# Performance work log

Hardware: AMD Instinct MI355X
Metric: run time of the kernel (lower is better)

The kernel has to match this reference:

```python
import jax, jax.numpy as jnp
import numpy as np

LOG2 = float(np.log(2.0))
CUTOFF = 10.0
N, E, H, F, G = 50000, 800000, 64, 64, 50


def ssp(x):
    # ShiftedSoftplus
    return jax.nn.softplus(x) - LOG2


def setup_inputs() -> dict:
    key = jax.random.key(0)
    ks = jax.random.split(key, 20)
    s = 0.05
    inp = {
        'x0': jax.random.normal(ks[0], (N, H), jnp.float32),
        'x1': jax.random.normal(ks[1], (N, H), jnp.float32),
        'edge_index0': jax.random.randint(ks[2], (2, E), 0, N, jnp.int32),
        'edge_index1': jax.random.randint(ks[3], (2, E), 0, N, jnp.int32),
        'edge_weight0': jax.random.uniform(ks[4], (E,), jnp.float32) * CUTOFF,
        'edge_weight1': jax.random.uniform(ks[5], (E,), jnp.float32) * CUTOFF,
        'edge_attr0': jax.random.uniform(ks[6], (E, G), jnp.float32),
        'edge_attr1': jax.random.uniform(ks[7], (E, G), jnp.float32),
        # shared filter MLP (num_gaussians -> num_filters -> num_filters)
        'mlp_w1': jax.random.normal(ks[8], (G, F), jnp.float32) * s,
        'mlp_b1': jnp.zeros((F,), jnp.float32),
        'mlp_w2': jax.random.normal(ks[9], (F, F), jnp.float32) * s,
        'mlp_b2': jnp.zeros((F,), jnp.float32),
        # per-edge-type CFConv lin1 (H->F, no bias) and lin2 (F->H, bias)
        'lin1_w0': jax.random.normal(ks[10], (H, F), jnp.float32) * s,
        'lin2_w0': jax.random.normal(ks[11], (F, H), jnp.float32) * s,
        'lin2_b0': jnp.zeros((H,), jnp.float32),
        'lin1_w1': jax.random.normal(ks[12], (H, F), jnp.float32) * s,
        'lin2_w1': jax.random.normal(ks[13], (F, H), jnp.float32) * s,
        'lin2_b1': jnp.zeros((H,), jnp.float32),
        # trailing shared linear H->H
        'lin_w': jax.random.normal(ks[14], (H, H), jnp.float32) * s,
        'lin_b': jnp.zeros((H,), jnp.float32),
    }
    return inp


def cfconv(x, ei, ew, ea, l1w, l2w, l2b, mw1, mb1, mw2, mb2):
    # cosine cutoff on distances
    C = 0.5 * (jnp.cos(ew * (jnp.pi / CUTOFF)) + 1.0)  # [E]
    # filter MLP on RBF edge attrs: Linear -> SSP -> Linear
    W = (ssp(ea @ mw1 + mb1) @ mw2 + mb2) * C[:, None]  # [E,F]
    xs = x @ l1w                                        # [N,F]
    msg = xs[ei[0]] * W                                 # gather src, modulate
    agg = jax.ops.segment_sum(msg, ei[1], num_segments=x.shape[0])  # scatter-sum to dst
    return agg @ l2w + l2b                              # [N,H]


def reference(x0, x1, edge_index0, edge_index1, edge_weight0, edge_weight1,
              edge_attr0, edge_attr1, mlp_w1, mlp_b1, mlp_w2, mlp_b2,
              lin1_w0, lin2_w0, lin2_b0, lin1_w1, lin2_w1, lin2_b1,
              lin_w, lin_b):
    h0 = cfconv(x0, edge_index0, edge_weight0, edge_attr0,
                lin1_w0, lin2_w0, lin2_b0, mlp_w1, mlp_b1, mlp_w2, mlp_b2)
    h1 = cfconv(x1, edge_index1, edge_weight1, edge_attr1,
                lin1_w1, lin2_w1, lin2_b1, mlp_w1, mlp_b1, mlp_w2, mlp_b2)
    out0 = ssp(h0) @ lin_w + lin_b
    out1 = ssp(h1) @ lin_w + lin_b
    return out0, out1
```

## Files before the change

kernel.cpp:

```cpp
#include <hip/hip_runtime.h>
#include <math.h>

#define HD 64
#define GD 50
#define HALF 32
#define PAD 36

__device__ __forceinline__ float ssp_f(float x) {
    float ax = __builtin_fabsf(x);
    float e  = __expf(-ax);
    float sp = fmaxf(x, 0.0f) + __logf(1.0f + e);
    return sp - 0.69314718055994531f;
}

__global__ void __launch_bounds__(256) xs_kernel(const float* __restrict__ x,
                                                 const float* __restrict__ w,
                                                 float* __restrict__ xs,
                                                 float* __restrict__ agg, int N) {
    int wv = threadIdx.x >> 6;
    int j  = threadIdx.x & 63;
    int n  = blockIdx.x * 4 + wv;
    __shared__ float xr[4][64];
    if (n < N) xr[wv][j] = x[(size_t)n * HD + j];
    __syncthreads();
    if (n >= N) return;
    float acc = 0.0f;
#pragma unroll
    for (int k = 0; k < HD; ++k)
        acc = fmaf(xr[wv][k], w[k * HD + j], acc);
    xs[(size_t)n * HD + j] = acc;
    agg[(size_t)n * HD + j] = 0.0f;
}

#define EPW 64
#define WPB 2
__global__ void __launch_bounds__(WPB * 64, 4) edge_kernel(
        const float* __restrict__ ea, const float* __restrict__ ew,
        const int* __restrict__ ei, const float* __restrict__ xs,
        float* __restrict__ agg,
        const float* __restrict__ mw1, const float* __restrict__ mb1,
        const float* __restrict__ mw2, const float* __restrict__ mb2,
        int E) {
    const int wv   = threadIdx.x >> 6;
    const int lane = threadIdx.x & 63;
    const long ebase = ((long)blockIdx.x * WPB + wv) * EPW;

    __shared__ float wbuf[WPB][EPW * PAD];
    __shared__ int   sdst[WPB][EPW];
    __shared__ int   ssrc[WPB][EPW];

    long e = ebase + lane;
    bool valid = e < (long)E;
    long ec = valid ? e : (long)E - 1;

    const float2* ear2 = (const float2*)(ea + ec * GD);
    float h[HD];
#pragma unroll
    for (int f = 0; f < HD; ++f) h[f] = mb1[f];
    {
        float2 v = ear2[0];
        for (int gc = 0; gc < GD / 2; ++gc) {
            int gn = gc + 1 < GD / 2 ? gc + 1 : GD / 2 - 1;
            float2 vn = ear2[gn];
            const float* wr = mw1 + 2 * gc * HD;
#pragma unroll
            for (int f = 0; f < HD; ++f) h[f] = fmaf(v.x, wr[f], h[f]);
#pragma unroll
            for (int f = 0; f < HD; ++f) h[f] = fmaf(v.y, wr[HD + f], h[f]);
            v = vn;
        }
    }

    float* hrow = &wbuf[wv][lane * PAD];
#pragma unroll
    for (int q = 0; q < HALF / 4; ++q)
        *(float4*)(hrow + 4 * q) = make_float4(h[HALF + 4*q],     h[HALF + 4*q + 1],
                                               h[HALF + 4*q + 2], h[HALF + 4*q + 3]);

    float w[HD];
#pragma unroll
    for (int j = 0; j < HD; ++j) w[j] = mb2[j];

#pragma unroll
    for (int gb = 0; gb < HALF / 4; ++gb) {
        float s0 = ssp_f(h[4*gb + 0]);
        float s1 = ssp_f(h[4*gb + 1]);
        float s2 = ssp_f(h[4*gb + 2]);
        float s3 = ssp_f(h[4*gb + 3]);
        const float* wr = mw2 + 4 * gb * HD;
#pragma unroll
        for (int j = 0; j < HD; ++j) w[j] = fmaf(s0, wr[j], w[j]);
#pragma unroll
        for (int j = 0; j < HD; ++j) w[j] = fmaf(s1, wr[HD + j], w[j]);
#pragma unroll
        for (int j = 0; j < HD; ++j) w[j] = fmaf(s2, wr[2 * HD + j], w[j]);
#pragma unroll
        for (int j = 0; j < HD; ++j) w[j] = fmaf(s3, wr[3 * HD + j], w[j]);
    }

    {
        float4 hv = *(const float4*)(hrow);
        for (int gb = 0; gb < HALF / 4; ++gb) {
            int gn = gb + 1 < HALF / 4 ? gb + 1 : HALF / 4 - 1;
            float4 hn = *(const float4*)(hrow + 4 * gn);
            float s0 = ssp_f(hv.x), s1 = ssp_f(hv.y), s2 = ssp_f(hv.z), s3 = ssp_f(hv.w);
            const float* wr = mw2 + (HALF + 4 * gb) * HD;
#pragma unroll
            for (int j = 0; j < HD; ++j) w[j] = fmaf(s0, wr[j], w[j]);
#pragma unroll
            for (int j = 0; j < HD; ++j) w[j] = fmaf(s1, wr[HD + j], w[j]);
#pragma unroll
            for (int j = 0; j < HD; ++j) w[j] = fmaf(s2, wr[2 * HD + j], w[j]);
#pragma unroll
            for (int j = 0; j < HD; ++j) w[j] = fmaf(s3, wr[3 * HD + j], w[j]);
            hv = hn;
        }
    }

    float cw = 0.5f * (__cosf(ew[ec] * 0.31415926535897931f) + 1.0f);
    if (!valid) cw = 0.0f;

    sdst[wv][lane] = ei[(size_t)E + ec];
    ssrc[wv][lane] = ei[ec];

    const int c  = lane & 31;
    const int eh = lane & 32;

#pragma unroll
    for (int q = 0; q < HALF / 4; ++q)
        *(float4*)(hrow + 4 * q) = make_float4(w[4*q] * cw,     w[4*q + 1] * cw,
                                               w[4*q + 2] * cw, w[4*q + 3] * cw);
    __syncthreads();
    float xh[EPW / 2];
#pragma unroll
    for (int t = 0; t < EPW / 2; ++t) {
        int idx = t + eh;
        int dst = sdst[wv][idx];
        int src = ssrc[wv][idx];
        const float* xp = xs + (size_t)src * HD + c;
        float xlo = xp[0];
        xh[t] = xp[HALF];
        float m = xlo * wbuf[wv][idx * PAD + c];
        atomicAdd(&agg[(size_t)dst * HD + c], m);
    }
    __syncthreads();

#pragma unroll
    for (int q = 0; q < HALF / 4; ++q)
        *(float4*)(hrow + 4 * q) = make_float4(w[HALF + 4*q] * cw,     w[HALF + 4*q + 1] * cw,
                                               w[HALF + 4*q + 2] * cw, w[HALF + 4*q + 3] * cw);
    __syncthreads();
#pragma unroll
    for (int t = 0; t < EPW / 2; ++t) {
        int idx = t + eh;
        int dst = sdst[wv][idx];
        float m = xh[t] * wbuf[wv][idx * PAD + c];
        atomicAdd(&agg[(size_t)dst * HD + HALF + c], m);
    }
}

__global__ void __launch_bounds__(256) out_kernel(
        const float* __restrict__ agg,
        const float* __restrict__ l2w, const float* __restrict__ l2b,
        const float* __restrict__ lw, const float* __restrict__ lb,
        float* __restrict__ out, int N) {
    int wv = threadIdx.x >> 6;
    int j  = threadIdx.x & 63;
    int n  = blockIdx.x * 4 + wv;
    __shared__ float buf[4][64];
    bool ok = n < N;
    if (ok) buf[wv][j] = agg[(size_t)n * HD + j];
    __syncthreads();
    float h = l2b[j];
#pragma unroll
    for (int g = 0; g < HD; ++g)
        h = fmaf(buf[wv][g], l2w[g * HD + j], h);
    h = ssp_f(h);
    __syncthreads();
    buf[wv][j] = h;
    __syncthreads();
    float o = lb[j];
#pragma unroll
    for (int g = 0; g < HD; ++g)
        o = fmaf(buf[wv][g], lw[g * HD + j], o);
    if (ok) out[(size_t)n * HD + j] = o;
}

extern "C" void kernel_launch(void* const* d_in, const int* in_sizes, int n_in,
                              void* d_out, int out_size, void* d_ws, size_t ws_size,
                              hipStream_t stream) {
    const float* x0   = (const float*)d_in[0];
    const float* x1   = (const float*)d_in[1];
    const int*   ei0  = (const int*)d_in[2];
    const int*   ei1  = (const int*)d_in[3];
    const float* ew0  = (const float*)d_in[4];
    const float* ew1  = (const float*)d_in[5];
    const float* ea0  = (const float*)d_in[6];
    const float* ea1  = (const float*)d_in[7];
    const float* mw1  = (const float*)d_in[8];
    const float* mb1  = (const float*)d_in[9];
    const float* mw2  = (const float*)d_in[10];
    const float* mb2  = (const float*)d_in[11];
    const float* l1w0 = (const float*)d_in[12];
    const float* l2w0 = (const float*)d_in[13];
    const float* l2b0 = (const float*)d_in[14];
    const float* l1w1 = (const float*)d_in[15];
    const float* l2w1 = (const float*)d_in[16];
    const float* l2b1 = (const float*)d_in[17];
    const float* lw   = (const float*)d_in[18];
    const float* lb   = (const float*)d_in[19];

    int N = in_sizes[0] / HD;
    int E = in_sizes[4];
    float* out = (float*)d_out;

    float* xs  = (float*)d_ws;
    float* agg = xs + (size_t)N * HD;

    int nodeBlocks = (N + 3) / 4;
    int edgeBlocks = (E + WPB * EPW - 1) / (WPB * EPW);

    for (int t = 0; t < 2; ++t) {
        const float* x   = t ? x1 : x0;
        const int*   ei  = t ? ei1 : ei0;
        const float* ew  = t ? ew1 : ew0;
        const float* ea  = t ? ea1 : ea0;
        const float* l1w = t ? l1w1 : l1w0;
        const float* l2w = t ? l2w1 : l2w0;
        const float* l2b = t ? l2b1 : l2b0;
        float* outp = out + (size_t)t * (size_t)N * HD;

        xs_kernel<<<nodeBlocks, 256, 0, stream>>>(x, l1w, xs, agg, N);
        edge_kernel<<<edgeBlocks, WPB * 64, 0, stream>>>(ea, ew, ei, xs, agg,
                                                         mw1, mb1, mw2, mb2, E);
        out_kernel<<<nodeBlocks, 256, 0, stream>>>(agg, l2w, l2b, lw, lb, outp, N);
    }
}
```

Before: 1.256 ms.

## Batch both edge types per launch and fuse filter MLP layers per column block

Merges the two CFConv passes into single launches with blockIdx.y selecting the edge type, so each kernel runs once over twice the work, provided the workspace is large enough. Inside the edge kernel, the RBF row is held in registers and the first MLP layer is computed four hidden units at a time, each followed immediately by its SSP and accumulation into the second layer. This drops the 64-element hidden array and its shared-memory spill, lowering register pressure. The cost is reloading mw1 for each column block, and the merged path needs a workspace sized for both node sets.

New measurement: 2.113 ms. 1.68x slower.

```diff
diff --git a/kernel.cpp b/kernel.cpp
--- a/kernel.cpp
+++ b/kernel.cpp
@@ -5,6 +5,8 @@
 #define GD 50
 #define HALF 32
 #define PAD 36
+#define EPW 64
+#define WPB 2
 
 __device__ __forceinline__ float ssp_f(float x) {
     float ax = __builtin_fabsf(x);
@@ -13,10 +15,19 @@
     return sp - 0.69314718055994531f;
 }
 
-__global__ void __launch_bounds__(256) xs_kernel(const float* __restrict__ x,
-                                                 const float* __restrict__ w,
-                                                 float* __restrict__ xs,
-                                                 float* __restrict__ agg, int N) {
+__global__ void __launch_bounds__(256) xs_kernel(
+        const float* __restrict__ xA, const float* __restrict__ xB,
+        const float* __restrict__ wA, const float* __restrict__ wB,
+        float* __restrict__ xsA, float* __restrict__ xsB,
+        float* __restrict__ aggA, float* __restrict__ aggB,
+        int NA, int NB) {
+    const int t = blockIdx.y;
+    const float* x   = t ? xB : xA;
+    const float* w   = t ? wB : wA;
+    float* xs  = t ? xsB : xsA;
+    float* agg = t ? aggB : aggA;
+    const int N = t ? NB : NA;
+
     int wv = threadIdx.x >> 6;
     int j  = threadIdx.x & 63;
     int n  = blockIdx.x * 4 + wv;
@@ -32,96 +43,93 @@
     agg[(size_t)n * HD + j] = 0.0f;
 }
 
-#define EPW 64
-#define WPB 2
 __global__ void __launch_bounds__(WPB * 64, 4) edge_kernel(
-        const float* __restrict__ ea, const float* __restrict__ ew,
-        const int* __restrict__ ei, const float* __restrict__ xs,
-        float* __restrict__ agg,
+        const float* __restrict__ eaA, const float* __restrict__ eaB,
+        const float* __restrict__ ewA, const float* __restrict__ ewB,
+        const int* __restrict__ eiA, const int* __restrict__ eiB,
+        const float* __restrict__ xsA, const float* __restrict__ xsB,
+        float* __restrict__ aggA, float* __restrict__ aggB,
         const float* __restrict__ mw1, const float* __restrict__ mb1,
         const float* __restrict__ mw2, const float* __restrict__ mb2,
-        int E) {
+        int EA, int EB) {
+    const int t = blockIdx.y;
+    const float* ea = t ? eaB : eaA;
+    const float* ew = t ? ewB : ewA;
+    const int*   ei = t ? eiB : eiA;
+    const float* xs = t ? xsB : xsA;
+    float*      agg = t ? aggB : aggA;
+    const int E = t ? EB : EA;
+
+    if ((size_t)blockIdx.x * (WPB * EPW) >= (size_t)E) return;
+
     const int wv   = threadIdx.x >> 6;
     const int lane = threadIdx.x & 63;
-    const long ebase = ((long)blockIdx.x * WPB + wv) * EPW;
+    const int ebase = (blockIdx.x * WPB + wv) * EPW;
 
     __shared__ float wbuf[WPB][EPW * PAD];
     __shared__ int   sdst[WPB][EPW];
     __shared__ int   ssrc[WPB][EPW];
 
-    long e = ebase + lane;
-    bool valid = e < (long)E;
-    long ec = valid ? e : (long)E - 1;
-
-    const float2* ear2 = (const float2*)(ea + ec * GD);
-    float h[HD];
-#pragma unroll
-    for (int f = 0; f < HD; ++f) h[f] = mb1[f];
-    {
-        float2 v = ear2[0];
-        for (int gc = 0; gc < GD / 2; ++gc) {
-            int gn = gc + 1 < GD / 2 ? gc + 1 : GD / 2 - 1;
-            float2 vn = ear2[gn];
-            const float* wr = mw1 + 2 * gc * HD;
-#pragma unroll
-            for (int f = 0; f < HD; ++f) h[f] = fmaf(v.x, wr[f], h[f]);
-#pragma unroll
-            for (int f = 0; f < HD; ++f) h[f] = fmaf(v.y, wr[HD + f], h[f]);
-            v = vn;
-        }
-    }
-
-    float* hrow = &wbuf[wv][lane * PAD];
-#pragma unroll
-    for (int q = 0; q < HALF / 4; ++q)
-        *(float4*)(hrow + 4 * q) = make_float4(h[HALF + 4*q],     h[HALF + 4*q + 1],
-                                               h[HALF + 4*q + 2], h[HALF + 4*q + 3]);
-
-    float w[HD];
-#pragma unroll
-    for (int j = 0; j < HD; ++j) w[j] = mb2[j];
-
-#pragma unroll
-    for (int gb = 0; gb < HALF / 4; ++gb) {
-        float s0 = ssp_f(h[4*gb + 0]);
-        float s1 = ssp_f(h[4*gb + 1]);
-        float s2 = ssp_f(h[4*gb + 2]);
-        float s3 = ssp_f(h[4*gb + 3]);
-        const float* wr = mw2 + 4 * gb * HD;
-#pragma unroll
-        for (int j = 0; j < HD; ++j) w[j] = fmaf(s0, wr[j], w[j]);
-#pragma unroll
-        for (int j = 0; j < HD; ++j) w[j] = fmaf(s1, wr[HD + j], w[j]);
-#pragma unroll
-        for (int j = 0; j < HD; ++j) w[j] = fmaf(s2, wr[2 * HD + j], w[j]);
-#pragma unroll
-        for (int j = 0; j < HD; ++j) w[j] = fmaf(s3, wr[3 * HD + j], w[j]);
-    }
-
-    {
-        float4 hv = *(const float4*)(hrow);
-        for (int gb = 0; gb < HALF / 4; ++gb) {
-            int gn = gb + 1 < HALF / 4 ? gb + 1 : HALF / 4 - 1;
-            float4 hn = *(const float4*)(hrow + 4 * gn);
-            float s0 = ssp_f(hv.x), s1 = ssp_f(hv.y), s2 = ssp_f(hv.z), s3 = ssp_f(hv.w);
-            const float* wr = mw2 + (HALF + 4 * gb) * HD;
-#pragma unroll
-            for (int j = 0; j < HD; ++j) w[j] = fmaf(s0, wr[j], w[j]);
-#pragma unroll
-            for (int j = 0; j < HD; ++j) w[j] = fmaf(s1, wr[HD + j], w[j]);
-#pragma unroll
-            for (int j = 0; j < HD; ++j) w[j] = fmaf(s2, wr[2 * HD + j], w[j]);
-#pragma unroll
-            for (int j = 0; j < HD; ++j) w[j] = fmaf(s3, wr[3 * HD + j], w[j]);
-            hv = hn;
-        }
-    }
-
+    int e = ebase + lane;
+    bool valid = e < E;
+    int ec = valid ? e : E - 1;
+
+    sdst[wv][lane] = ei[(size_t)E + ec];
+    ssrc[wv][lane] = ei[ec];
     float cw = 0.5f * (__cosf(ew[ec] * 0.31415926535897931f) + 1.0f);
     if (!valid) cw = 0.0f;
 
-    sdst[wv][lane] = ei[(size_t)E + ec];
-    ssrc[wv][lane] = ei[ec];
+    const float2* ear2 = (const float2*)(ea + (size_t)ec * GD);
+    float2 re[23];
+#pragma unroll
+    for (int g = 0; g < 23; ++g) re[g] = ear2[g];
+    float2 rt0 = ear2[23], rt1 = ear2[24];
+    float* hrow = &wbuf[wv][lane * PAD];
+    *(float4*)(hrow + HALF) = make_float4(rt0.x, rt0.y, rt1.x, rt1.y);
+
+    float w[HD];
+#pragma unroll
+    for (int j = 0; j < HD; ++j) w[j] = mb2[j];
+
+#pragma unroll 2
+    for (int cb = 0; cb < HD / 4; ++cb) {
+        const int c0 = 4 * cb;
+        float h0 = mb1[c0], h1 = mb1[c0 + 1], h2 = mb1[c0 + 2], h3 = mb1[c0 + 3];
+#pragma unroll
+        for (int g = 0; g < 23; ++g) {
+            const float* w0 = mw1 + (2 * g) * HD + c0;
+            h0 = fmaf(re[g].x, w0[0], h0);
+            h1 = fmaf(re[g].x, w0[1], h1);
+            h2 = fmaf(re[g].x, w0[2], h2);
+            h3 = fmaf(re[g].x, w0[3], h3);
+            h0 = fmaf(re[g].y, w0[HD],     h0);
+            h1 = fmaf(re[g].y, w0[HD + 1], h1);
+            h2 = fmaf(re[g].y, w0[HD + 2], h2);
+            h3 = fmaf(re[g].y, w0[HD + 3], h3);
+        }
+        {
+            float4 rt = *(const float4*)(hrow + HALF);
+            const float* w0 = mw1 + 46 * HD + c0;
+            h0 = fmaf(rt.x, w0[0], h0); h1 = fmaf(rt.x, w0[1], h1);
+            h2 = fmaf(rt.x, w0[2], h2); h3 = fmaf(rt.x, w0[3], h3);
+            h0 = fmaf(rt.y, w0[HD],     h0); h1 = fmaf(rt.y, w0[HD + 1], h1);
+            h2 = fmaf(rt.y, w0[HD + 2], h2); h3 = fmaf(rt.y, w0[HD + 3], h3);
+            h0 = fmaf(rt.z, w0[2*HD],     h0); h1 = fmaf(rt.z, w0[2*HD + 1], h1);
+            h2 = fmaf(rt.z, w0[2*HD + 2], h2); h3 = fmaf(rt.z, w0[2*HD + 3], h3);
+            h0 = fmaf(rt.w, w0[3*HD],     h0); h1 = fmaf(rt.w, w0[3*HD + 1], h1);
+            h2 = fmaf(rt.w, w0[3*HD + 2], h2); h3 = fmaf(rt.w, w0[3*HD + 3], h3);
+        }
+        float s0 = ssp_f(h0), s1 = ssp_f(h1), s2 = ssp_f(h2), s3 = ssp_f(h3);
+        const float* r0 = mw2 + c0 * HD;
+#pragma unroll
+        for (int j = 0; j < HD; ++j) w[j] = fmaf(s0, r0[j], w[j]);
+#pragma unroll
+        for (int j = 0; j < HD; ++j) w[j] = fmaf(s1, r0[HD + j], w[j]);
+#pragma unroll
+        for (int j = 0; j < HD; ++j) w[j] = fmaf(s2, r0[2 * HD + j], w[j]);
+#pragma unroll
+        for (int j = 0; j < HD; ++j) w[j] = fmaf(s3, r0[3 * HD + j], w[j]);
+    }
 
     const int c  = lane & 31;
     const int eh = lane & 32;
@@ -133,15 +141,14 @@
     __syncthreads();
     float xh[EPW / 2];
 #pragma unroll
-    for (int t = 0; t < EPW / 2; ++t) {
-        int idx = t + eh;
+    for (int k = 0; k < EPW / 2; ++k) {
+        int idx = k + eh;
         int dst = sdst[wv][idx];
         int src = ssrc[wv][idx];
         const float* xp = xs + (size_t)src * HD + c;
         float xlo = xp[0];
-        xh[t] = xp[HALF];
-        float m = xlo * wbuf[wv][idx * PAD + c];
-        atomicAdd(&agg[(size_t)dst * HD + c], m);
+        xh[k] = xp[HALF];
+        atomicAdd(&agg[(size_t)dst * HD + c], xlo * wbuf[wv][idx * PAD + c]);
     }
     __syncthreads();
 
@@ -151,19 +158,27 @@
                                                w[HALF + 4*q + 2] * cw, w[HALF + 4*q + 3] * cw);
     __syncthreads();
 #pragma unroll
-    for (int t = 0; t < EPW / 2; ++t) {
-        int idx = t + eh;
+    for (int k = 0; k < EPW / 2; ++k) {
+        int idx = k + eh;
         int dst = sdst[wv][idx];
-        float m = xh[t] * wbuf[wv][idx * PAD + c];
-        atomicAdd(&agg[(size_t)dst * HD + HALF + c], m);
+        atomicAdd(&agg[(size_t)dst * HD + HALF + c], xh[k] * wbuf[wv][idx * PAD + c]);
     }
 }
 
 __global__ void __launch_bounds__(256) out_kernel(
-        const float* __restrict__ agg,
-        const float* __restrict__ l2w, const float* __restrict__ l2b,
+        const float* __restrict__ aggA, const float* __restrict__ aggB,
+        const float* __restrict__ l2wA, const float* __restrict__ l2wB,
+        const float* __restrict__ l2bA, const float* __restrict__ l2bB,
         const float* __restrict__ lw, const float* __restrict__ lb,
-        float* __restrict__ out, int N) {
+        float* __restrict__ outA, float* __restrict__ outB,
+        int NA, int NB) {
+    const int t = blockIdx.y;
+    const float* agg = t ? aggB : aggA;
+    const float* l2w = t ? l2wB : l2wA;
+    const float* l2b = t ? l2bB : l2bA;
+    float* out = t ? outB : outA;
+    const int N = t ? NB : NA;
+
     int wv = threadIdx.x >> 6;
     int j  = threadIdx.x & 63;
     int n  = blockIdx.x * 4 + wv;
@@ -210,29 +225,57 @@
     const float* lw   = (const float*)d_in[18];
     const float* lb   = (const float*)d_in[19];
 
-    int N = in_sizes[0] / HD;
-    int E = in_sizes[4];
+    int N0 = in_sizes[0] / HD;
+    int N1 = in_sizes[1] / HD;
+    int E0 = in_sizes[4];
+    int E1 = in_sizes[5];
     float* out = (float*)d_out;
-
-    float* xs  = (float*)d_ws;
-    float* agg = xs + (size_t)N * HD;
-
-    int nodeBlocks = (N + 3) / 4;
-    int edgeBlocks = (E + WPB * EPW - 1) / (WPB * EPW);
-
-    for (int t = 0; t < 2; ++t) {
-        const float* x   = t ? x1 : x0;
-        const int*   ei  = t ? ei1 : ei0;
-        const float* ew  = t ? ew1 : ew0;
-        const float* ea  = t ? ea1 : ea0;
-        const float* l1w = t ? l1w1 : l1w0;
-        const float* l2w = t ? l2w1 : l2w0;
-        const float* l2b = t ? l2b1 : l2b0;
-        float* outp = out + (size_t)t * (size_t)N * HD;
-
-        xs_kernel<<<nodeBlocks, 256, 0, stream>>>(x, l1w, xs, agg, N);
-        edge_kernel<<<edgeBlocks, WPB * 64, 0, stream>>>(ea, ew, ei, xs, agg,
-                                                         mw1, mb1, mw2, mb2, E);
-        out_kernel<<<nodeBlocks, 256, 0, stream>>>(agg, l2w, l2b, lw, lb, outp, N);
-    }
-}
+    float* out0 = out;
+    float* out1 = out + (size_t)N0 * HD;
+
+    int Nmax = N0 > N1 ? N0 : N1;
+    int Emax = E0 > E1 ? E0 : E1;
+    int nodeBlocks = (Nmax + 3) / 4;
+    int edgeBlocks = (Emax + WPB * EPW - 1) / (WPB * EPW);
+
+    size_t needMerged = (size_t)(N0 + N1) * HD * 2 * sizeof(float);
+
+    if (ws_size >= needMerged) {
+        float* xs0  = (float*)d_ws;
+        float* xs1  = xs0 + (size_t)N0 * HD;
+        float* agg0 = xs1 + (size_t)N1 * HD;
+        float* agg1 = agg0 + (size_t)N0 * HD;
+
+        xs_kernel<<<dim3(nodeBlocks, 2), 256, 0, stream>>>(
+            x0, x1, l1w0, l1w1, xs0, xs1, agg0, agg1, N0, N1);
+        edge_kernel<<<dim3(edgeBlocks, 2), WPB * 64, 0, stream>>>(
+            ea0, ea1, ew0, ew1, ei0, ei1, xs0, xs1, agg0, agg1,
+            mw1, mb1, mw2, mb2, E0, E1);
+        out_kernel<<<dim3(nodeBlocks, 2), 256, 0, stream>>>(
+            agg0, agg1, l2w0, l2w1, l2b0, l2b1, lw, lb, out0, out1, N0, N1);
+    } else {
+        float* xs  = (float*)d_ws;
+        float* agg = xs + (size_t)Nmax * HD;
+        for (int t = 0; t < 2; ++t) {
+            const float* x   = t ? x1 : x0;
+            const int*   ei  = t ? ei1 : ei0;
+            const float* ewp = t ? ew1 : ew0;
+            const float* eap = t ? ea1 : ea0;
+            const float* l1w = t ? l1w1 : l1w0;
+            const float* l2w = t ? l2w1 : l2w0;
+            const float* l2b = t ? l2b1 : l2b0;
+            int N = t ? N1 : N0;
+            int E = t ? E1 : E0;
+            float* outp = t ? out1 : out0;
+            int nb = (N + 3) / 4;
+            int eb = (E + WPB * EPW - 1) / (WPB * EPW);
+            xs_kernel<<<dim3(nb, 1), 256, 0, stream>>>(
+                x, x, l1w, l1w, xs, xs, agg, agg, N, N);
+            edge_kernel<<<dim3(eb, 1), WPB * 64, 0, stream>>>(
+                eap, eap, ewp, ewp, ei, ei, xs, xs, agg, agg,
+                mw1, mb1, mw2, mb2, E, E);
+            out_kernel<<<dim3(nb, 1), 256, 0, stream>>>(
+                agg, agg, l2w, l2w, l2b, l2b, lw, lb, outp, outp, N, N);
+        }
+    }
+}
```
